# Performance work log

Hardware: AMD Instinct MI355X
Metric: run time of the kernel (lower is better)

## Reference

```python
import jax, jax.numpy as jnp
import numpy as np

B_PAIR = 4      # anchor/positive pairs; total batch = 2*B_PAIR
NUM = 4096      # keypoints per cloud
C_FEAT = 640    # descriptor dim
NB_ITER = 5


def _rigid_transform(a, b, weights):
    # a: (B,M,3), b: (B,M,3), weights: (B,M) -> (B,3,4)
    wn = weights[..., None] / (jnp.sum(weights[..., None], axis=1, keepdims=True) + 1e-5)
    centroid_a = jnp.sum(a * wn, axis=1)            # (B,3)
    centroid_b = jnp.sum(b * wn, axis=1)
    a_c = a - centroid_a[:, None, :]
    b_c = b - centroid_b[:, None, :]
    cov = jnp.swapaxes(a_c, -2, -1) @ (b_c * wn)    # (B,3,3)
    u, s, vh = jnp.linalg.svd(cov, full_matrices=False)
    v = jnp.swapaxes(vh, -2, -1)                    # torch.svd returns v, jax returns vh
    rot_pos = v @ jnp.swapaxes(u, -2, -1)
    v_neg = v.at[:, :, 2].multiply(-1.0)
    rot_neg = v_neg @ jnp.swapaxes(u, -2, -1)
    rot = jnp.where(jnp.linalg.det(rot_pos)[:, None, None] > 0, rot_pos, rot_neg)
    trans = -rot @ centroid_a[:, :, None] + centroid_b[:, :, None]
    return jnp.concatenate((rot, trans), axis=2)    # (B,3,4)


def _uot_forward(point_features, point_coords, gamma, epsilon):
    feats = point_features[..., 0]                  # (2B, C, N)
    twoB, _, N = feats.shape
    B = twoB // 2
    feat1 = jnp.transpose(feats[:B], (0, 2, 1))     # (B, N, C)
    feat2 = jnp.transpose(feats[B:], (0, 2, 1))
    coords = point_coords.reshape(twoB, -1, 4)
    coords1 = coords[:B, :, 1:]                     # (B, N, 3)
    coords2 = coords[B:, :, 1:]

    eps = jnp.exp(epsilon) + 0.03                   # scalar (1,)
    gam = jnp.exp(gamma)

    f1 = feat1 / jnp.sqrt(jnp.sum(feat1**2, -1, keepdims=True) + 1e-8)
    f2 = feat2 / jnp.sqrt(jnp.sum(feat2**2, -1, keepdims=True) + 1e-8)
    Cmat = 1.0 - jnp.einsum('bnc,bmc->bnm', f1, f2)  # (B,N,N) cosine cost
    K = jnp.exp(-Cmat / eps)

    power = gam / (gam + eps)
    inv_n = jnp.asarray(1.0 / N, K.dtype)
    a = jnp.full((B, N, 1), inv_n, K.dtype)
    prob1 = jnp.full((B, N, 1), inv_n, K.dtype)
    prob2 = jnp.full((B, N, 1), inv_n, K.dtype)
    b = prob2
    for _ in range(NB_ITER):                        # unrolled unbalanced Sinkhorn
        KTa = jnp.matmul(jnp.swapaxes(K, 1, 2), a)  # (B,N,1)
        b = jnp.power(prob2 / (KTa + 1e-8), power)
        Kb = jnp.matmul(K, b)
        a = jnp.power(prob1 / (Kb + 1e-8), power)
    T = a * K * jnp.swapaxes(b, 1, 2)               # (B,N,N) transport plan

    row_sum = jnp.sum(T, axis=-1, keepdims=True)    # (B,N,1)
    sinkhorn_matches = jnp.matmul(T, coords2) / (row_sum + 1e-8)  # (B,N,3)
    transform = _rigid_transform(coords1, sinkhorn_matches, row_sum[..., 0])
    return T, sinkhorn_matches, transform


def setup_inputs() -> dict:
    key = jax.random.key(0)
    k1, k2 = jax.random.split(key)
    point_features = jax.random.normal(k1, (2 * B_PAIR, C_FEAT, NUM, 1), dtype=jnp.float32)
    point_coords = jax.random.normal(k2, (2 * B_PAIR * NUM, 4), dtype=jnp.float32) * 10.0
    gamma = jnp.zeros((1,), jnp.float32)
    epsilon = jnp.zeros((1,), jnp.float32)
    return {"point_features": point_features, "point_coords": point_coords,
            "gamma": gamma, "epsilon": epsilon}


def reference(point_features, point_coords, gamma, epsilon):
    return _uot_forward(point_features, point_coords, gamma, epsilon)
```

## Files before the change

### kernel.cpp

```cpp
#include <hip/hip_runtime.h>
#include <math.h>

#define NB 4
#define N 4096
#define CF 640

typedef _Float16 f16;
typedef _Float16 f16x8 __attribute__((ext_vector_type(8)));
typedef _Float16 f16x4 __attribute__((ext_vector_type(4)));
typedef float    f32x4 __attribute__((ext_vector_type(4)));
typedef unsigned int u32;

#define OFF_FNT   0ll
#define OFF_RNORM (OFF_FNT + 8ll*N*CF*2)
#define OFF_BVEC  (OFF_RNORM + 8ll*N*4)
#define OFF_SCR   (OFF_BVEC + (long long)NB*N*4)
#define OFF_KTAP  (OFF_SCR + (long long)NB*N*N*2)
#define REQ_H     (OFF_KTAP + (long long)NB*64*N*4)
#define REQ_F     (OFF_SCR + (long long)NB*64*N*4)

__device__ inline void async_copy16(void* lds, const void* g) {
    __builtin_amdgcn_global_load_lds(
        (const __attribute__((address_space(1))) u32*)g,
        (__attribute__((address_space(3))) u32*)lds,
        16, 0, 0);
}

__global__ __launch_bounds__(256) void rnorm_kernel(const float* __restrict__ pf,
                                                    float* __restrict__ rnorm) {
    int idx = blockIdx.x * 256 + threadIdx.x;
    int n = idx & (N - 1);
    int b = idx >> 12;
    const float* src = pf + (size_t)b * CF * N + n;
    float s = 0.f;
    for (int c = 0; c < CF; ++c) { float v = src[(size_t)c * N]; s = fmaf(v, v, s); }
    rnorm[idx] = 1.0f / sqrtf(s + 1e-8f);
}

__global__ __launch_bounds__(256) void transpose_kernel(const float* __restrict__ pf,
                                                        const float* __restrict__ rnorm,
                                                        f16* __restrict__ fnT) {
    __shared__ float tile[64][65];
    int b  = blockIdx.z;
    int c0 = blockIdx.x * 64;
    int n1 = blockIdx.y * 64;
    int t  = threadIdx.x;

    int c_l = t >> 4;
    int n_l4 = (t & 15) * 4;
    #pragma unroll
    for (int i = 0; i < 4; ++i) {
        int c = c_l + i * 16;
        float4 v = *(const float4*)(pf + (size_t)(b * CF + c0 + c) * N + n1 + n_l4);
        tile[c][n_l4 + 0] = v.x; tile[c][n_l4 + 1] = v.y;
        tile[c][n_l4 + 2] = v.z; tile[c][n_l4 + 3] = v.w;
    }
    __syncthreads();

    int n_l = t >> 2;
    int c_g = (t & 3) * 16;
    float rn = rnorm[b * N + n1 + n_l];
    f16 tmp[16] __attribute__((aligned(16)));
    #pragma unroll
    for (int i = 0; i < 16; ++i)
        tmp[i] = (f16)(tile[c_g + i][n_l] * rn);
    f16* dst = fnT + (size_t)(b * N + n1 + n_l) * CF + c0 + c_g;
    ((uint4*)dst)[0] = ((const uint4*)tmp)[0];
    ((uint4*)dst)[1] = ((const uint4*)tmp)[1];
}

template<bool H>
__global__ __launch_bounds__(256) void gemm_k(const f16* __restrict__ fnT,
                                              const float* __restrict__ e_in,
                                              float* __restrict__ Kf,
                                              f16* __restrict__ Kh,
                                              float* __restrict__ ktap) {
    int b  = blockIdx.z;
    int m0 = blockIdx.y * 128;
    int n0 = blockIdx.x * 128;
    const f16* A = fnT + (size_t)b       * N * CF;
    const f16* B = fnT + (size_t)(b + 4) * N * CF;

    __shared__ f16 As[128 * 32];
    __shared__ f16 Bs[128 * 32];
    __shared__ float cs[2][128];
    __shared__ f16 Ct[H ? 128 * 136 : 1];

    int tid = threadIdx.x;
    int w = tid >> 6;
    int l = tid & 63;
    int wr = w >> 1, wc = w & 1;

    f32x4 acc[4][4];
    #pragma unroll
    for (int i = 0; i < 4; ++i)
        #pragma unroll
        for (int j = 0; j < 4; ++j)
            acc[i][j] = (f32x4){0.f, 0.f, 0.f, 0.f};

    int srow = l >> 2;
    int scp  = l & 3;

    for (int c0 = 0; c0 < CF; c0 += 32) {
        #pragma unroll
        for (int q = 0; q < 2; ++q) {
            int ch = w * 2 + q;
            int row = ch * 16 + srow;
            int cc = scp ^ ((row >> 1) & 3);
            async_copy16(&As[ch * 512], A + (size_t)(n0 + row) * CF + c0 + cc * 8);
            async_copy16(&Bs[ch * 512], B + (size_t)(m0 + row) * CF + c0 + cc * 8);
        }
        __syncthreads();

        f16x8 af[4], bfr[4];
        int g = l >> 4, low = l & 15;
        #pragma unroll
        for (int t = 0; t < 4; ++t) {
            int rowA = wr * 64 + t * 16 + low;
            af[t] = *(const f16x8*)(As + rowA * 32 + (g ^ ((rowA >> 1) & 3)) * 8);
            int rowB = wc * 64 + t * 16 + low;
            bfr[t] = *(const f16x8*)(Bs + rowB * 32 + (g ^ ((rowB >> 1) & 3)) * 8);
        }
        #pragma unroll
        for (int i = 0; i < 4; ++i)
            #pragma unroll
            for (int j = 0; j < 4; ++j)
                acc[i][j] = __builtin_amdgcn_mfma_f32_16x16x32_f16(af[i], bfr[j], acc[i][j], 0, 0, 0);
        __syncthreads();
    }

    float eps = expf(e_in[0]) + 0.03f;
    float inv_eps = 1.0f / eps;
    int g4 = l >> 4, low = l & 15;
    float colp[4] = {0.f, 0.f, 0.f, 0.f};
    float* out = Kf + (size_t)b * N * N;

    #pragma unroll
    for (int i = 0; i < 4; ++i) {
        int rl = wr * 64 + i * 16 + g4 * 4;
        #pragma unroll
        for (int j = 0; j < 4; ++j) {
            int cl = wc * 64 + j * 16 + low;
            #pragma unroll
            for (int r = 0; r < 4; ++r) {
                float v = expf((acc[i][j][r] - 1.0f) * inv_eps);
                out[(size_t)(n0 + rl + r) * N + m0 + cl] = v;
                if constexpr (H) Ct[(rl + r) * 136 + cl] = (f16)v;
                colp[j] += v;
            }
        }
    }

    #pragma unroll
    for (int j = 0; j < 4; ++j) {
        float c = colp[j];
        c += __shfl_down(c, 32);
        c += __shfl_down(c, 16);
        if (l < 16) cs[wr][wc * 64 + j * 16 + l] = c;
    }
    __syncthreads();
    if (tid < 128)
        ktap[((size_t)b * 64 + blockIdx.x) * N + m0 + tid] =
            (cs[0][tid] + cs[1][tid]) * (1.0f / N);

    if constexpr (H) {
        f16* oh = Kh + (size_t)b * N * N;
        int row0 = tid >> 4, c8 = (tid & 15) * 8;
        #pragma unroll
        for (int rr = 0; rr < 8; ++rr) {
            int row = rr * 16 + row0;
            f16x8 v = *(const f16x8*)(Ct + row * 136 + c8);
            *(f16x8*)(oh + (size_t)(n0 + row) * N + m0 + c8) = v;
        }
    }
}

__global__ __launch_bounds__(256) void bvec_kernel(const float* __restrict__ ktap,
                                                   int npart, int slotstride,
                                                   const float* __restrict__ g_in,
                                                   const float* __restrict__ e_in,
                                                   float* __restrict__ bvec) {
    int cl = threadIdx.x & 63;
    int pg = threadIdx.x >> 6;
    int i = blockIdx.x * 64 + cl;
    int b = i >> 12, m = i & (N - 1);
    const float* p = ktap + (size_t)b * slotstride * N + m;
    int per = npart >> 2;
    float s = 0.f;
    #pragma unroll 8
    for (int k = pg * per; k < (pg + 1) * per; ++k) s += p[(size_t)k * N];
    __shared__ float sh[4][64];
    sh[pg][cl] = s; __syncthreads();
    if (threadIdx.x < 64) {
        float tot = sh[0][cl] + sh[1][cl] + sh[2][cl] + sh[3][cl];
        float eps = expf(e_in[0]) + 0.03f;
        float gam = expf(g_in[0]);
        float power = gam / (gam + eps);
        bvec[i] = powf((1.0f / N) / (tot + 1e-8f), power);
    }
}

template<bool H>
__global__ __launch_bounds__(256) void fused_iter(const void* __restrict__ Kp,
                                                  const float* __restrict__ bv_in,
                                                  const float* __restrict__ g_in,
                                                  const float* __restrict__ e_in,
                                                  float* __restrict__ ktap) {
    int b = blockIdx.y, slab = blockIdx.x;
    int n0s = slab * 16;
    int w = threadIdx.x >> 6, l = threadIdx.x & 63;
    __shared__ float ash[16];
    float eps = expf(e_in[0]) + 0.03f;
    float gam = expf(g_in[0]);
    float power = gam / (gam + eps);
    const float* bv = bv_in + b * N;

    float acc[4] = {0.f, 0.f, 0.f, 0.f};

    if constexpr (H) {
        const f16* Kb = (const f16*)Kp + ((size_t)b * N + n0s) * N;
        for (int it = 0; it < 8; ++it) {
            int m = it * 512 + l * 8;
            float bq[8];
            *(float4*)&bq[0] = *(const float4*)(bv + m);
            *(float4*)&bq[4] = *(const float4*)(bv + m + 4);
            #pragma unroll
            for (int rr = 0; rr < 4; ++rr) {
                f16x8 v = *(const f16x8*)(Kb + (size_t)(w * 4 + rr) * N + m);
                #pragma unroll
                for (int q = 0; q < 8; ++q) acc[rr] = fmaf((float)v[q], bq[q], acc[rr]);
            }
        }
    } else {
        const float* Kb = (const float*)Kp + ((size_t)b * N + n0s) * N;
        for (int it = 0; it < 16; ++it) {
            int m = it * 256 + l * 4;
            float4 bq = *(const float4*)(bv + m);
            #pragma unroll
            for (int rr = 0; rr < 4; ++rr) {
                float4 v = *(const float4*)(Kb + (size_t)(rr * 4 + w) * N + m);
                acc[rr] = fmaf(v.x, bq.x, acc[rr]);
                acc[rr] = fmaf(v.y, bq.y, acc[rr]);
                acc[rr] = fmaf(v.z, bq.z, acc[rr]);
                acc[rr] = fmaf(v.w, bq.w, acc[rr]);
            }
        }
    }
    #pragma unroll
    for (int rr = 0; rr < 4; ++rr) {
        float s = acc[rr];
        s += __shfl_down(s, 32);
        s += __shfl_down(s, 16);
        s += __shfl_down(s, 8);
        s += __shfl_down(s, 4);
        s += __shfl_down(s, 2);
        s += __shfl_down(s, 1);
        if (l == 0) ash[(H ? w * 4 + rr : rr * 4 + w)] =
            powf((1.0f / N) / (s + 1e-8f), power);
    }
    __syncthreads();

    float cacc[16];
    #pragma unroll
    for (int q = 0; q < 16; ++q) cacc[q] = 0.f;
    int t4 = threadIdx.x * 4;
    if constexpr (H) {
        const f16* Kb = (const f16*)Kp + ((size_t)b * N + n0s) * N;
        for (int r = 0; r < 16; ++r) {
            float a = ash[r];
            #pragma unroll
            for (int q = 0; q < 4; ++q) {
                f16x4 v = *(const f16x4*)(Kb + (size_t)r * N + q * 1024 + t4);
                #pragma unroll
                for (int j = 0; j < 4; ++j)
                    cacc[q * 4 + j] = fmaf((float)v[j], a, cacc[q * 4 + j]);
            }
        }
    } else {
        const float* Kb = (const float*)Kp + ((size_t)b * N + n0s) * N;
        for (int r = 0; r < 16; ++r) {
            float a = ash[r];
            #pragma unroll
            for (int q = 0; q < 4; ++q) {
                float4 v = *(const float4*)(Kb + (size_t)r * N + q * 1024 + t4);
                cacc[q * 4 + 0] = fmaf(v.x, a, cacc[q * 4 + 0]);
                cacc[q * 4 + 1] = fmaf(v.y, a, cacc[q * 4 + 1]);
                cacc[q * 4 + 2] = fmaf(v.z, a, cacc[q * 4 + 2]);
                cacc[q * 4 + 3] = fmaf(v.w, a, cacc[q * 4 + 3]);
            }
        }
    }
    float* o = ktap + ((size_t)b * 256 + slab) * N;
    #pragma unroll
    for (int q = 0; q < 4; ++q)
        *(float4*)(o + q * 1024 + t4) =
            make_float4(cacc[q * 4], cacc[q * 4 + 1], cacc[q * 4 + 2], cacc[q * 4 + 3]);
}

__global__ __launch_bounds__(256) void final_k(float* __restrict__ Tout,
                                               const float* __restrict__ bv_in,
                                               const float* __restrict__ g_in,
                                               const float* __restrict__ e_in,
                                               const float* __restrict__ pc,
                                               float* __restrict__ rowsum,
                                               float* __restrict__ matches) {
    int b = blockIdx.y, n = blockIdx.x;
    int t = threadIdx.x;
    int t4 = t * 4;
    const float* bv = bv_in + b * N;
    float kv[16], bl[16];
    float* Trow = Tout + ((size_t)b * N + n) * N;
    #pragma unroll
    for (int q = 0; q < 4; ++q) {
        *(float4*)&bl[q * 4] = *(const float4*)(bv + q * 1024 + t4);
        *(float4*)&kv[q * 4] = *(const float4*)(Trow + q * 1024 + t4);
    }
    float s = 0.f;
    #pragma unroll
    for (int q = 0; q < 16; ++q) s = fmaf(kv[q], bl[q], s);
    __shared__ float red[256];
    red[t] = s; __syncthreads();
    for (int off = 128; off; off >>= 1) {
        if (t < off) red[t] += red[t + off];
        __syncthreads();
    }
    __shared__ float a_sh;
    if (t == 0) {
        float eps = expf(e_in[0]) + 0.03f;
        float gam = expf(g_in[0]);
        float power = gam / (gam + eps);
        a_sh = powf((1.0f / N) / (red[0] + 1e-8f), power);
    }
    __syncthreads();
    float an = a_sh;
    const float4* c2 = (const float4*)pc + (size_t)(4 + b) * N;
    float rs = 0.f, s0 = 0.f, s1 = 0.f, s2 = 0.f;
    #pragma unroll
    for (int q = 0; q < 4; ++q) {
        float tv0 = an * kv[q * 4 + 0] * bl[q * 4 + 0];
        float tv1 = an * kv[q * 4 + 1] * bl[q * 4 + 1];
        float tv2 = an * kv[q * 4 + 2] * bl[q * 4 + 2];
        float tv3 = an * kv[q * 4 + 3] * bl[q * 4 + 3];
        *(float4*)(Trow + q * 1024 + t4) = make_float4(tv0, tv1, tv2, tv3);
        rs += tv0 + tv1 + tv2 + tv3;
        float4 c0 = c2[q * 1024 + t4],     c1 = c2[q * 1024 + t4 + 1],
               cc = c2[q * 1024 + t4 + 2], c3 = c2[q * 1024 + t4 + 3];
        s0 = fmaf(tv0, c0.y, s0); s1 = fmaf(tv0, c0.z, s1); s2 = fmaf(tv0, c0.w, s2);
        s0 = fmaf(tv1, c1.y, s0); s1 = fmaf(tv1, c1.z, s1); s2 = fmaf(tv1, c1.w, s2);
        s0 = fmaf(tv2, cc.y, s0); s1 = fmaf(tv2, cc.z, s1); s2 = fmaf(tv2, cc.w, s2);
        s0 = fmaf(tv3, c3.y, s0); s1 = fmaf(tv3, c3.z, s1); s2 = fmaf(tv3, c3.w, s2);
    }
    __shared__ float4 red4[256];
    red4[t] = make_float4(rs, s0, s1, s2); __syncthreads();
    for (int off = 128; off; off >>= 1) {
        if (t < off) {
            float4 o = red4[t + off];
            red4[t].x += o.x; red4[t].y += o.y; red4[t].z += o.z; red4[t].w += o.w;
        }
        __syncthreads();
    }
    if (t == 0) {
        float4 tot = red4[0];
        rowsum[b * N + n] = tot.x;
        float inv = 1.0f / (tot.x + 1e-8f);
        float* mo = matches + ((size_t)b * N + n) * 3;
        mo[0] = tot.y * inv; mo[1] = tot.z * inv; mo[2] = tot.w * inv;
    }
}

__global__ __launch_bounds__(256) void transform_kernel(const float* __restrict__ rowsum,
                                                        const float* __restrict__ matches,
                                                        const float* __restrict__ pc,
                                                        float* __restrict__ out) {
    int b = blockIdx.x;
    float vals[16];
    #pragma unroll
    for (int q = 0; q < 16; ++q) vals[q] = 0.f;
    for (int n = threadIdx.x; n < N; n += 256) {
        float w = rowsum[b * N + n];
        float4 c1 = ((const float4*)pc)[(size_t)b * N + n];
        float ax = c1.y, ay = c1.z, az = c1.w;
        const float* mm = matches + ((size_t)b * N + n) * 3;
        float bx = mm[0], by = mm[1], bz = mm[2];
        vals[0] += w;
        vals[1] = fmaf(w, ax, vals[1]); vals[2] = fmaf(w, ay, vals[2]); vals[3] = fmaf(w, az, vals[3]);
        vals[4] = fmaf(w, bx, vals[4]); vals[5] = fmaf(w, by, vals[5]); vals[6] = fmaf(w, bz, vals[6]);
        vals[7]  = fmaf(w * ax, bx, vals[7]);  vals[8]  = fmaf(w * ax, by, vals[8]);  vals[9]  = fmaf(w * ax, bz, vals[9]);
        vals[10] = fmaf(w * ay, bx, vals[10]); vals[11] = fmaf(w * ay, by, vals[11]); vals[12] = fmaf(w * ay, bz, vals[12]);
        vals[13] = fmaf(w * az, bx, vals[13]); vals[14] = fmaf(w * az, by, vals[14]); vals[15] = fmaf(w * az, bz, vals[15]);
    }
    __shared__ float red[256];
    __shared__ float tot[16];
    for (int q = 0; q < 16; ++q) {
        red[threadIdx.x] = vals[q]; __syncthreads();
        for (int off = 128; off; off >>= 1) {
            if (threadIdx.x < off) red[threadIdx.x] += red[threadIdx.x + off];
            __syncthreads();
        }
        if (threadIdx.x == 0) tot[q] = red[0];
        __syncthreads();
    }
    if (threadIdx.x != 0) return;

    double S = tot[0];
    double denom = S + 1e-5;
    double Ca[3], Cb[3], M[3][3], cov[3][3];
    for (int i = 0; i < 3; ++i) { Ca[i] = tot[1 + i] / denom; Cb[i] = tot[4 + i] / denom; }
    for (int i = 0; i < 3; ++i)
        for (int j = 0; j < 3; ++j)
            M[i][j] = tot[7 + i * 3 + j] / denom;
    double s0 = S / denom;
    for (int i = 0; i < 3; ++i)
        for (int j = 0; j < 3; ++j)
            cov[i][j] = M[i][j] - Ca[i] * Cb[j] * (2.0 - s0);

    double Sm[3][3], V[3][3] = {{1,0,0},{0,1,0},{0,0,1}};
    for (int i = 0; i < 3; ++i)
        for (int j = 0; j < 3; ++j) {
            double acc = 0;
            for (int k = 0; k < 3; ++k) acc += cov[k][i] * cov[k][j];
            Sm[i][j] = acc;
        }
    for (int sweep = 0; sweep < 20; ++sweep) {
        static const int pq[3][2] = {{0,1},{0,2},{1,2}};
        for (int r = 0; r < 3; ++r) {
            int p = pq[r][0], q = pq[r][1];
            double apq = Sm[p][q];
            if (fabs(apq) < 1e-30) continue;
            double tau = (Sm[q][q] - Sm[p][p]) / (2.0 * apq);
            double t = (tau >= 0) ? 1.0 / (tau + sqrt(1.0 + tau * tau))
                                  : 1.0 / (tau - sqrt(1.0 + tau * tau));
            double c = 1.0 / sqrt(1.0 + t * t), s = t * c;
            for (int i = 0; i < 3; ++i) {
                double sip = Sm[i][p], siq = Sm[i][q];
                Sm[i][p] = c * sip - s * siq; Sm[i][q] = s * sip + c * siq;
            }
            for (int j = 0; j < 3; ++j) {
                double spj = Sm[p][j], sqj = Sm[q][j];
                Sm[p][j] = c * spj - s * sqj; Sm[q][j] = s * spj + c * sqj;
            }
            for (int i = 0; i < 3; ++i) {
                double vip = V[i][p], viq = V[i][q];
                V[i][p] = c * vip - s * viq; V[i][q] = s * vip + c * viq;
            }
        }
    }
    double lam[3] = {Sm[0][0], Sm[1][1], Sm[2][2]};
    for (int i = 0; i < 2; ++i)
        for (int j = i + 1; j < 3; ++j)
            if (lam[j] > lam[i]) {
                double tl = lam[i]; lam[i] = lam[j]; lam[j] = tl;
                for (int k = 0; k < 3; ++k) { double tv = V[k][i]; V[k][i] = V[k][j]; V[k][j] = tv; }
            }
    double U[3][3];
    double sig0 = sqrt(fmax(lam[0], 0.0));
    for (int j = 0; j < 3; ++j) {
        double sig = sqrt(fmax(lam[j], 0.0));
        if (sig > 1e-12 * (sig0 + 1e-300)) {
            double nrm = 0;
            for (int i = 0; i < 3; ++i) {
                double u = cov[i][0] * V[0][j] + cov[i][1] * V[1][j] + cov[i][2] * V[2][j];
                U[i][j] = u; nrm += u * u;
            }
            nrm = 1.0 / sqrt(nrm + 1e-300);
            for (int i = 0; i < 3; ++i) U[i][j] *= nrm;
        } else {
            U[0][j] = U[1][0] * U[2][1] - U[2][0] * U[1][1];
            U[1][j] = U[2][0] * U[0][1] - U[0][0] * U[2][1];
            U[2][j] = U[0][0] * U[1][1] - U[1][0] * U[0][1];
        }
    }
    double R[3][3];
    for (int i = 0; i < 3; ++i)
        for (int j = 0; j < 3; ++j)
            R[i][j] = V[i][0] * U[j][0] + V[i][1] * U[j][1] + V[i][2] * U[j][2];
    double det = R[0][0] * (R[1][1] * R[2][2] - R[1][2] * R[2][1])
               - R[0][1] * (R[1][0] * R[2][2] - R[1][2] * R[2][0])
               + R[0][2] * (R[1][0] * R[2][1] - R[1][1] * R[2][0]);
    if (!(det > 0)) {
        for (int k = 0; k < 3; ++k) V[k][2] = -V[k][2];
        for (int i = 0; i < 3; ++i)
            for (int j = 0; j < 3; ++j)
                R[i][j] = V[i][0] * U[j][0] + V[i][1] * U[j][1] + V[i][2] * U[j][2];
    }
    double tr[3];
    for (int i = 0; i < 3; ++i)
        tr[i] = -(R[i][0] * Ca[0] + R[i][1] * Ca[1] + R[i][2] * Ca[2]) + Cb[i];
    float* o = out + b * 12;
    for (int i = 0; i < 3; ++i) {
        o[i * 4 + 0] = (float)R[i][0];
        o[i * 4 + 1] = (float)R[i][1];
        o[i * 4 + 2] = (float)R[i][2];
        o[i * 4 + 3] = (float)tr[i];
    }
}

extern "C" void kernel_launch(void* const* d_in, const int* in_sizes, int n_in,
                              void* d_out, int out_size, void* d_ws, size_t ws_size,
                              hipStream_t stream) {
    const float* pf   = (const float*)d_in[0];
    const float* pc   = (const float*)d_in[1];
    const float* g_in = (const float*)d_in[2];
    const float* e_in = (const float*)d_in[3];

    char* wsb = (char*)d_ws;
    f16*   fnT   = (f16*)(wsb + OFF_FNT);
    float* rnorm = (float*)(wsb + OFF_RNORM);
    float* bvec  = (float*)(wsb + OFF_BVEC);

    float* T_out   = (float*)d_out;
    float* matches = T_out + (size_t)NB * N * N;
    float* trans   = matches + (size_t)NB * N * 3;
    float* rowsum  = rnorm;

    rnorm_kernel<<<dim3(8 * N / 256), 256, 0, stream>>>(pf, rnorm);
    transpose_kernel<<<dim3(CF / 64, N / 64, 8), 256, 0, stream>>>(pf, rnorm, fnT);

    float* ktapF = (float*)(wsb + OFF_FNT);

    if (ws_size >= (size_t)REQ_H) {
        f16*   Kh    = (f16*)(wsb + OFF_SCR);
        float* ktapG = (float*)(wsb + OFF_KTAP);
        gemm_k<true><<<dim3(N / 128, N / 128, NB), 256, 0, stream>>>(fnT, e_in, T_out, Kh, ktapG);
        bvec_kernel<<<dim3(NB * N / 64), 256, 0, stream>>>(ktapG, 32, 64, g_in, e_in, bvec);
        for (int it = 0; it < 4; ++it) {
            fused_iter<true><<<dim3(N / 16, NB), 256, 0, stream>>>(Kh, bvec, g_in, e_in, ktapF);
            bvec_kernel<<<dim3(NB * N / 64), 256, 0, stream>>>(ktapF, 256, 256, g_in, e_in, bvec);
        }
        final_k<<<dim3(N, NB), 256, 0, stream>>>(T_out, bvec, g_in, e_in, pc, rowsum, matches);
    } else {
        float* ktapG = (float*)(wsb + OFF_SCR);
        gemm_k<false><<<dim3(N / 128, N / 128, NB), 256, 0, stream>>>(fnT, e_in, T_out, (f16*)nullptr, ktapG);
        bvec_kernel<<<dim3(NB * N / 64), 256, 0, stream>>>(ktapG, 32, 64, g_in, e_in, bvec);
        for (int it = 0; it < 4; ++it) {
            fused_iter<false><<<dim3(N / 16, NB), 256, 0, stream>>>(T_out, bvec, g_in, e_in, ktapF);
            bvec_kernel<<<dim3(NB * N / 64), 256, 0, stream>>>(ktapF, 256, 256, g_in, e_in, bvec);
        }
        final_k<<<dim3(N, NB), 256, 0, stream>>>(T_out, bvec, g_in, e_in, pc, rowsum, matches);
    }

    transform_kernel<<<dim3(NB), 256, 0, stream>>>(rowsum, matches, pc, trans);
}
```

Baseline: 867.6 us.

## Keep K slab in registers across Sinkhorn halves and batch final rows

```diff
diff --git a/kernel.cpp b/kernel.cpp
--- a/kernel.cpp
+++ b/kernel.cpp
@@ -24,6 +24,16 @@
         (const __attribute__((address_space(1))) u32*)g,
         (__attribute__((address_space(3))) u32*)lds,
         16, 0, 0);
+}
+
+__device__ inline float wave_sum(float s) {
+    s += __shfl_down(s, 32);
+    s += __shfl_down(s, 16);
+    s += __shfl_down(s, 8);
+    s += __shfl_down(s, 4);
+    s += __shfl_down(s, 2);
+    s += __shfl_down(s, 1);
+    return s;
 }
 
 __global__ __launch_bounds__(256) void rnorm_kernel(const float* __restrict__ pf,
@@ -84,7 +94,7 @@
     __shared__ f16 As[128 * 32];
     __shared__ f16 Bs[128 * 32];
     __shared__ float cs[2][128];
-    __shared__ f16 Ct[H ? 128 * 136 : 1];
+    __shared__ f16 Ct[H ? 64 * 136 : 1];
 
     int tid = threadIdx.x;
     int w = tid >> 6;
@@ -145,7 +155,7 @@
             for (int r = 0; r < 4; ++r) {
                 float v = expf((acc[i][j][r] - 1.0f) * inv_eps);
                 out[(size_t)(n0 + rl + r) * N + m0 + cl] = v;
-                if constexpr (H) Ct[(rl + r) * 136 + cl] = (f16)v;
+                acc[i][j][r] = v;
                 colp[j] += v;
             }
         }
@@ -165,12 +175,30 @@
 
     if constexpr (H) {
         f16* oh = Kh + (size_t)b * N * N;
-        int row0 = tid >> 4, c8 = (tid & 15) * 8;
-        #pragma unroll
-        for (int rr = 0; rr < 8; ++rr) {
-            int row = rr * 16 + row0;
-            f16x8 v = *(const f16x8*)(Ct + row * 136 + c8);
-            *(f16x8*)(oh + (size_t)(n0 + row) * N + m0 + c8) = v;
+        int row0 = tid >> 4, c8v = (tid & 15) * 8;
+        #pragma unroll
+        for (int half = 0; half < 2; ++half) {
+            __syncthreads();
+            if (wr == half) {
+                #pragma unroll
+                for (int i = 0; i < 4; ++i) {
+                    int rl = i * 16 + g4 * 4;
+                    #pragma unroll
+                    for (int j = 0; j < 4; ++j) {
+                        int cl = wc * 64 + j * 16 + low;
+                        #pragma unroll
+                        for (int r = 0; r < 4; ++r)
+                            Ct[(rl + r) * 136 + cl] = (f16)acc[i][j][r];
+                    }
+                }
+            }
+            __syncthreads();
+            #pragma unroll
+            for (int rr = 0; rr < 4; ++rr) {
+                int row = rr * 16 + row0;
+                f16x8 v = *(const f16x8*)(Ct + row * 136 + c8v);
+                *(f16x8*)(oh + (size_t)(n0 + half * 64 + row) * N + m0 + c8v) = v;
+            }
         }
     }
 }
@@ -208,93 +236,112 @@
                                                   float* __restrict__ ktap) {
     int b = blockIdx.y, slab = blockIdx.x;
     int n0s = slab * 16;
-    int w = threadIdx.x >> 6, l = threadIdx.x & 63;
-    __shared__ float ash[16];
+    int t = threadIdx.x;
+    int w = t >> 6, l = t & 63;
+    __shared__ float wred[4][4];
     float eps = expf(e_in[0]) + 0.03f;
     float gam = expf(g_in[0]);
     float power = gam / (gam + eps);
     const float* bv = bv_in + b * N;
 
-    float acc[4] = {0.f, 0.f, 0.f, 0.f};
-
     if constexpr (H) {
+        float bl[16];
+        #pragma unroll
+        for (int q = 0; q < 2; ++q) {
+            *(float4*)&bl[q * 8]     = *(const float4*)(bv + q * 2048 + t * 8);
+            *(float4*)&bl[q * 8 + 4] = *(const float4*)(bv + q * 2048 + t * 8 + 4);
+        }
+        float cacc[16];
+        #pragma unroll
+        for (int q = 0; q < 16; ++q) cacc[q] = 0.f;
         const f16* Kb = (const f16*)Kp + ((size_t)b * N + n0s) * N;
-        for (int it = 0; it < 8; ++it) {
-            int m = it * 512 + l * 8;
-            float bq[8];
-            *(float4*)&bq[0] = *(const float4*)(bv + m);
-            *(float4*)&bq[4] = *(const float4*)(bv + m + 4);
-            #pragma unroll
-            for (int rr = 0; rr < 4; ++rr) {
-                f16x8 v = *(const f16x8*)(Kb + (size_t)(w * 4 + rr) * N + m);
+
+        for (int g4 = 0; g4 < 4; ++g4) {
+            f16x8 kr[4][2];
+            #pragma unroll
+            for (int r = 0; r < 4; ++r)
                 #pragma unroll
-                for (int q = 0; q < 8; ++q) acc[rr] = fmaf((float)v[q], bq[q], acc[rr]);
-            }
+                for (int q = 0; q < 2; ++q)
+                    kr[r][q] = *(const f16x8*)(Kb + (size_t)(g4 * 4 + r) * N + q * 2048 + t * 8);
+            #pragma unroll
+            for (int r = 0; r < 4; ++r) {
+                float s = 0.f;
+                #pragma unroll
+                for (int q = 0; q < 2; ++q)
+                    #pragma unroll
+                    for (int j = 0; j < 8; ++j)
+                        s = fmaf((float)kr[r][q][j], bl[q * 8 + j], s);
+                s = wave_sum(s);
+                if (l == 0) wred[w][r] = s;
+            }
+            __syncthreads();
+            float av[4];
+            #pragma unroll
+            for (int r = 0; r < 4; ++r) {
+                float s = wred[0][r] + wred[1][r] + wred[2][r] + wred[3][r];
+                av[r] = powf((1.0f / N) / (s + 1e-8f), power);
+            }
+            __syncthreads();
+            #pragma unroll
+            for (int r = 0; r < 4; ++r)
+                #pragma unroll
+                for (int q = 0; q < 2; ++q)
+                    #pragma unroll
+                    for (int j = 0; j < 8; ++j)
+                        cacc[q * 8 + j] = fmaf((float)kr[r][q][j], av[r], cacc[q * 8 + j]);
+        }
+        float* o = ktap + ((size_t)b * 256 + slab) * N;
+        #pragma unroll
+        for (int q = 0; q < 2; ++q) {
+            *(float4*)(o + q * 2048 + t * 8)     = make_float4(cacc[q*8+0], cacc[q*8+1], cacc[q*8+2], cacc[q*8+3]);
+            *(float4*)(o + q * 2048 + t * 8 + 4) = make_float4(cacc[q*8+4], cacc[q*8+5], cacc[q*8+6], cacc[q*8+7]);
         }
     } else {
+        int t4 = t * 4;
+        float bl[16];
+        #pragma unroll
+        for (int q = 0; q < 4; ++q)
+            *(float4*)&bl[q * 4] = *(const float4*)(bv + q * 1024 + t4);
+        float cacc[16];
+        #pragma unroll
+        for (int q = 0; q < 16; ++q) cacc[q] = 0.f;
         const float* Kb = (const float*)Kp + ((size_t)b * N + n0s) * N;
-        for (int it = 0; it < 16; ++it) {
-            int m = it * 256 + l * 4;
-            float4 bq = *(const float4*)(bv + m);
-            #pragma unroll
-            for (int rr = 0; rr < 4; ++rr) {
-                float4 v = *(const float4*)(Kb + (size_t)(rr * 4 + w) * N + m);
-                acc[rr] = fmaf(v.x, bq.x, acc[rr]);
-                acc[rr] = fmaf(v.y, bq.y, acc[rr]);
-                acc[rr] = fmaf(v.z, bq.z, acc[rr]);
-                acc[rr] = fmaf(v.w, bq.w, acc[rr]);
-            }
-        }
-    }
-    #pragma unroll
-    for (int rr = 0; rr < 4; ++rr) {
-        float s = acc[rr];
-        s += __shfl_down(s, 32);
-        s += __shfl_down(s, 16);
-        s += __shfl_down(s, 8);
-        s += __shfl_down(s, 4);
-        s += __shfl_down(s, 2);
-        s += __shfl_down(s, 1);
-        if (l == 0) ash[(H ? w * 4 + rr : rr * 4 + w)] =
-            powf((1.0f / N) / (s + 1e-8f), power);
-    }
-    __syncthreads();
-
-    float cacc[16];
-    #pragma unroll
-    for (int q = 0; q < 16; ++q) cacc[q] = 0.f;
-    int t4 = threadIdx.x * 4;
-    if constexpr (H) {
-        const f16* Kb = (const f16*)Kp + ((size_t)b * N + n0s) * N;
-        for (int r = 0; r < 16; ++r) {
-            float a = ash[r];
-            #pragma unroll
-            for (int q = 0; q < 4; ++q) {
-                f16x4 v = *(const f16x4*)(Kb + (size_t)r * N + q * 1024 + t4);
+
+        for (int g4 = 0; g4 < 4; ++g4) {
+            float kr[4][16];
+            #pragma unroll
+            for (int r = 0; r < 4; ++r)
                 #pragma unroll
-                for (int j = 0; j < 4; ++j)
-                    cacc[q * 4 + j] = fmaf((float)v[j], a, cacc[q * 4 + j]);
-            }
-        }
-    } else {
-        const float* Kb = (const float*)Kp + ((size_t)b * N + n0s) * N;
-        for (int r = 0; r < 16; ++r) {
-            float a = ash[r];
-            #pragma unroll
-            for (int q = 0; q < 4; ++q) {
-                float4 v = *(const float4*)(Kb + (size_t)r * N + q * 1024 + t4);
-                cacc[q * 4 + 0] = fmaf(v.x, a, cacc[q * 4 + 0]);
-                cacc[q * 4 + 1] = fmaf(v.y, a, cacc[q * 4 + 1]);
-                cacc[q * 4 + 2] = fmaf(v.z, a, cacc[q * 4 + 2]);
-                cacc[q * 4 + 3] = fmaf(v.w, a, cacc[q * 4 + 3]);
-            }
-        }
-    }
-    float* o = ktap + ((size_t)b * 256 + slab) * N;
-    #pragma unroll
-    for (int q = 0; q < 4; ++q)
-        *(float4*)(o + q * 1024 + t4) =
-            make_float4(cacc[q * 4], cacc[q * 4 + 1], cacc[q * 4 + 2], cacc[q * 4 + 3]);
+                for (int q = 0; q < 4; ++q)
+                    *(float4*)&kr[r][q * 4] = *(const float4*)(Kb + (size_t)(g4 * 4 + r) * N + q * 1024 + t4);
+            #pragma unroll
+            for (int r = 0; r < 4; ++r) {
+                float s = 0.f;
+                #pragma unroll
+                for (int q = 0; q < 16; ++q) s = fmaf(kr[r][q], bl[q], s);
+                s = wave_sum(s);
+                if (l == 0) wred[w][r] = s;
+            }
+            __syncthreads();
+            float av[4];
+            #pragma unroll
+            for (int r = 0; r < 4; ++r) {
+                float s = wred[0][r] + wred[1][r] + wred[2][r] + wred[3][r];
+                av[r] = powf((1.0f / N) / (s + 1e-8f), power);
+            }
+            __syncthreads();
+            #pragma unroll
+            for (int r = 0; r < 4; ++r)
+                #pragma unroll
+                for (int q = 0; q < 16; ++q)
+                    cacc[q] = fmaf(kr[r][q], av[r], cacc[q]);
+        }
+        float* o = ktap + ((size_t)b * 256 + slab) * N;
+        #pragma unroll
+        for (int q = 0; q < 4; ++q)
+            *(float4*)(o + q * 1024 + t4) =
+                make_float4(cacc[q * 4], cacc[q * 4 + 1], cacc[q * 4 + 2], cacc[q * 4 + 3]);
+    }
 }
 
 __global__ __launch_bounds__(256) void final_k(float* __restrict__ Tout,
@@ -304,66 +351,87 @@
                                                const float* __restrict__ pc,
                                                float* __restrict__ rowsum,
                                                float* __restrict__ matches) {
-    int b = blockIdx.y, n = blockIdx.x;
-    int t = threadIdx.x;
+    int b = blockIdx.y, n0r = blockIdx.x * 4;
+    int t = threadIdx.x, w = t >> 6, l = t & 63;
     int t4 = t * 4;
     const float* bv = bv_in + b * N;
-    float kv[16], bl[16];
-    float* Trow = Tout + ((size_t)b * N + n) * N;
-    #pragma unroll
-    for (int q = 0; q < 4; ++q) {
+    float eps = expf(e_in[0]) + 0.03f;
+    float gam = expf(g_in[0]);
+    float power = gam / (gam + eps);
+
+    float bl[16];
+    #pragma unroll
+    for (int q = 0; q < 4; ++q)
         *(float4*)&bl[q * 4] = *(const float4*)(bv + q * 1024 + t4);
-        *(float4*)&kv[q * 4] = *(const float4*)(Trow + q * 1024 + t4);
-    }
-    float s = 0.f;
-    #pragma unroll
-    for (int q = 0; q < 16; ++q) s = fmaf(kv[q], bl[q], s);
-    __shared__ float red[256];
-    red[t] = s; __syncthreads();
-    for (int off = 128; off; off >>= 1) {
-        if (t < off) red[t] += red[t + off];
-        __syncthreads();
-    }
-    __shared__ float a_sh;
-    if (t == 0) {
-        float eps = expf(e_in[0]) + 0.03f;
-        float gam = expf(g_in[0]);
-        float power = gam / (gam + eps);
-        a_sh = powf((1.0f / N) / (red[0] + 1e-8f), power);
+
+    float* Trow0 = Tout + ((size_t)b * N + n0r) * N;
+    float kv[4][16];
+    #pragma unroll
+    for (int r = 0; r < 4; ++r)
+        #pragma unroll
+        for (int q = 0; q < 4; ++q)
+            *(float4*)&kv[r][q * 4] = *(const float4*)(Trow0 + (size_t)r * N + q * 1024 + t4);
+
+    __shared__ float wred[4][4];
+    #pragma unroll
+    for (int r = 0; r < 4; ++r) {
+        float s = 0.f;
+        #pragma unroll
+        for (int q = 0; q < 16; ++q) s = fmaf(kv[r][q], bl[q], s);
+        s = wave_sum(s);
+        if (l == 0) wred[w][r] = s;
     }
     __syncthreads();
-    float an = a_sh;
+    float av[4];
+    #pragma unroll
+    for (int r = 0; r < 4; ++r) {
+        float s = wred[0][r] + wred[1][r] + wred[2][r] + wred[3][r];
+        av[r] = powf((1.0f / N) / (s + 1e-8f), power);
+    }
+
     const float4* c2 = (const float4*)pc + (size_t)(4 + b) * N;
-    float rs = 0.f, s0 = 0.f, s1 = 0.f, s2 = 0.f;
-    #pragma unroll
-    for (int q = 0; q < 4; ++q) {
-        float tv0 = an * kv[q * 4 + 0] * bl[q * 4 + 0];
-        float tv1 = an * kv[q * 4 + 1] * bl[q * 4 + 1];
-        float tv2 = an * kv[q * 4 + 2] * bl[q * 4 + 2];
-        float tv3 = an * kv[q * 4 + 3] * bl[q * 4 + 3];
-        *(float4*)(Trow + q * 1024 + t4) = make_float4(tv0, tv1, tv2, tv3);
-        rs += tv0 + tv1 + tv2 + tv3;
-        float4 c0 = c2[q * 1024 + t4],     c1 = c2[q * 1024 + t4 + 1],
-               cc = c2[q * 1024 + t4 + 2], c3 = c2[q * 1024 + t4 + 3];
-        s0 = fmaf(tv0, c0.y, s0); s1 = fmaf(tv0, c0.z, s1); s2 = fmaf(tv0, c0.w, s2);
-        s0 = fmaf(tv1, c1.y, s0); s1 = fmaf(tv1, c1.z, s1); s2 = fmaf(tv1, c1.w, s2);
-        s0 = fmaf(tv2, cc.y, s0); s1 = fmaf(tv2, cc.z, s1); s2 = fmaf(tv2, cc.w, s2);
-        s0 = fmaf(tv3, c3.y, s0); s1 = fmaf(tv3, c3.z, s1); s2 = fmaf(tv3, c3.w, s2);
-    }
-    __shared__ float4 red4[256];
-    red4[t] = make_float4(rs, s0, s1, s2); __syncthreads();
-    for (int off = 128; off; off >>= 1) {
-        if (t < off) {
-            float4 o = red4[t + off];
-            red4[t].x += o.x; red4[t].y += o.y; red4[t].z += o.z; red4[t].w += o.w;
-        }
-        __syncthreads();
-    }
-    if (t == 0) {
-        float4 tot = red4[0];
-        rowsum[b * N + n] = tot.x;
+    float rsv[4], s0v[4], s1v[4], s2v[4];
+    #pragma unroll
+    for (int r = 0; r < 4; ++r) {
+        float rs = 0.f, s0 = 0.f, s1 = 0.f, s2 = 0.f;
+        float an = av[r];
+        #pragma unroll
+        for (int q = 0; q < 4; ++q) {
+            int idx = q * 1024 + t4;
+            float tv0 = an * kv[r][q * 4 + 0] * bl[q * 4 + 0];
+            float tv1 = an * kv[r][q * 4 + 1] * bl[q * 4 + 1];
+            float tv2 = an * kv[r][q * 4 + 2] * bl[q * 4 + 2];
+            float tv3 = an * kv[r][q * 4 + 3] * bl[q * 4 + 3];
+            *(float4*)(Trow0 + (size_t)r * N + idx) = make_float4(tv0, tv1, tv2, tv3);
+            rs += tv0 + tv1 + tv2 + tv3;
+            float4 c0 = c2[idx], c1 = c2[idx + 1], cc = c2[idx + 2], c3 = c2[idx + 3];
+            s0 = fmaf(tv0, c0.y, s0); s1 = fmaf(tv0, c0.z, s1); s2 = fmaf(tv0, c0.w, s2);
+            s0 = fmaf(tv1, c1.y, s0); s1 = fmaf(tv1, c1.z, s1); s2 = fmaf(tv1, c1.w, s2);
+            s0 = fmaf(tv2, cc.y, s0); s1 = fmaf(tv2, cc.z, s1); s2 = fmaf(tv2, cc.w, s2);
+            s0 = fmaf(tv3, c3.y, s0); s1 = fmaf(tv3, c3.z, s1); s2 = fmaf(tv3, c3.w, s2);
+        }
+        rsv[r] = rs; s0v[r] = s0; s1v[r] = s1; s2v[r] = s2;
+    }
+
+    __shared__ float4 wred4[4][4];
+    #pragma unroll
+    for (int r = 0; r < 4; ++r) {
+        float rs = wave_sum(rsv[r]);
+        float s0 = wave_sum(s0v[r]);
+        float s1 = wave_sum(s1v[r]);
+        float s2 = wave_sum(s2v[r]);
+        if (l == 0) wred4[w][r] = make_float4(rs, s0, s1, s2);
+    }
+    __syncthreads();
+    if (t < 4) {
+        float4 a0 = wred4[0][t], a1 = wred4[1][t], a2 = wred4[2][t], a3 = wred4[3][t];
+        float4 tot = make_float4(a0.x + a1.x + a2.x + a3.x,
+                                 a0.y + a1.y + a2.y + a3.y,
+                                 a0.z + a1.z + a2.z + a3.z,
+                                 a0.w + a1.w + a2.w + a3.w);
+        rowsum[b * N + n0r + t] = tot.x;
         float inv = 1.0f / (tot.x + 1e-8f);
-        float* mo = matches + ((size_t)b * N + n) * 3;
+        float* mo = matches + ((size_t)b * N + n0r + t) * 3;
         mo[0] = tot.y * inv; mo[1] = tot.z * inv; mo[2] = tot.w * inv;
     }
 }
@@ -373,34 +441,34 @@
                                                         const float* __restrict__ pc,
                                                         float* __restrict__ out) {
     int b = blockIdx.x;
+    int t = threadIdx.x, w = t >> 6, l = t & 63;
     float vals[16];
     #pragma unroll
     for (int q = 0; q < 16; ++q) vals[q] = 0.f;
-    for (int n = threadIdx.x; n < N; n += 256) {
-        float w = rowsum[b * N + n];
+    for (int n = t; n < N; n += 256) {
+        float wgt = rowsum[b * N + n];
         float4 c1 = ((const float4*)pc)[(size_t)b * N + n];
         float ax = c1.y, ay = c1.z, az = c1.w;
         const float* mm = matches + ((size_t)b * N + n) * 3;
         float bx = mm[0], by = mm[1], bz = mm[2];
-        vals[0] += w;
-        vals[1] = fmaf(w, ax, vals[1]); vals[2] = fmaf(w, ay, vals[2]); vals[3] = fmaf(w, az, vals[3]);
-        vals[4] = fmaf(w, bx, vals[4]); vals[5] = fmaf(w, by, vals[5]); vals[6] = fmaf(w, bz, vals[6]);
-        vals[7]  = fmaf(w * ax, bx, vals[7]);  vals[8]  = fmaf(w * ax, by, vals[8]);  vals[9]  = fmaf(w * ax, bz, vals[9]);
-        vals[10] = fmaf(w * ay, bx, vals[10]); vals[11] = fmaf(w * ay, by, vals[11]); vals[12] = fmaf(w * ay, bz, vals[12]);
-        vals[13] = fmaf(w * az, bx, vals[13]); vals[14] = fmaf(w * az, by, vals[14]); vals[15] = fmaf(w * az, bz, vals[15]);
-    }
-    __shared__ float red[256];
+        vals[0] += wgt;
+        vals[1] = fmaf(wgt, ax, vals[1]); vals[2] = fmaf(wgt, ay, vals[2]); vals[3] = fmaf(wgt, az, vals[3]);
+        vals[4] = fmaf(wgt, bx, vals[4]); vals[5] = fmaf(wgt, by, vals[5]); vals[6] = fmaf(wgt, bz, vals[6]);
+        vals[7]  = fmaf(wgt * ax, bx, vals[7]);  vals[8]  = fmaf(wgt * ax, by, vals[8]);  vals[9]  = fmaf(wgt * ax, bz, vals[9]);
+        vals[10] = fmaf(wgt * ay, bx, vals[10]); vals[11] = fmaf(wgt * ay, by, vals[11]); vals[12] = fmaf(wgt * ay, bz, vals[12]);
+        vals[13] = fmaf(wgt * az, bx, vals[13]); vals[14] = fmaf(wgt * az, by, vals[14]); vals[15] = fmaf(wgt * az, bz, vals[15]);
+    }
+    __shared__ float sh[4][16];
     __shared__ float tot[16];
+    #pragma unroll
     for (int q = 0; q < 16; ++q) {
-        red[threadIdx.x] = vals[q]; __syncthreads();
-        for (int off = 128; off; off >>= 1) {
-            if (threadIdx.x < off) red[threadIdx.x] += red[threadIdx.x + off];
-            __syncthreads();
-        }
-        if (threadIdx.x == 0) tot[q] = red[0];
-        __syncthreads();
-    }
-    if (threadIdx.x != 0) return;
+        float s = wave_sum(vals[q]);
+        if (l == 0) sh[w][q] = s;
+    }
+    __syncthreads();
+    if (t < 16) tot[t] = sh[0][t] + sh[1][t] + sh[2][t] + sh[3][t];
+    __syncthreads();
+    if (t != 0) return;
 
     double S = tot[0];
     double denom = S + 1e-5;
@@ -428,9 +496,9 @@
             double apq = Sm[p][q];
             if (fabs(apq) < 1e-30) continue;
             double tau = (Sm[q][q] - Sm[p][p]) / (2.0 * apq);
-            double t = (tau >= 0) ? 1.0 / (tau + sqrt(1.0 + tau * tau))
-                                  : 1.0 / (tau - sqrt(1.0 + tau * tau));
-            double c = 1.0 / sqrt(1.0 + t * t), s = t * c;
+            double t2 = (tau >= 0) ? 1.0 / (tau + sqrt(1.0 + tau * tau))
+                                   : 1.0 / (tau - sqrt(1.0 + tau * tau));
+            double c = 1.0 / sqrt(1.0 + t2 * t2), s = t2 * c;
             for (int i = 0; i < 3; ++i) {
                 double sip = Sm[i][p], siq = Sm[i][q];
                 Sm[i][p] = c * sip - s * siq; Sm[i][q] = s * sip + c * siq;
@@ -527,7 +595,7 @@
             fused_iter<true><<<dim3(N / 16, NB), 256, 0, stream>>>(Kh, bvec, g_in, e_in, ktapF);
             bvec_kernel<<<dim3(NB * N / 64), 256, 0, stream>>>(ktapF, 256, 256, g_in, e_in, bvec);
         }
-        final_k<<<dim3(N, NB), 256, 0, stream>>>(T_out, bvec, g_in, e_in, pc, rowsum, matches);
+        final_k<<<dim3(N / 4, NB), 256, 0, stream>>>(T_out, bvec, g_in, e_in, pc, rowsum, matches);
     } else {
         float* ktapG = (float*)(wsb + OFF_SCR);
         gemm_k<false><<<dim3(N / 128, N / 128, NB), 256, 0, stream>>>(fnT, e_in, T_out, (f16*)nullptr, ktapG);
@@ -536,7 +604,7 @@
             fused_iter<false><<<dim3(N / 16, NB), 256, 0, stream>>>(T_out, bvec, g_in, e_in, ktapF);
             bvec_kernel<<<dim3(NB * N / 64), 256, 0, stream>>>(ktapF, 256, 256, g_in, e_in, bvec);
         }
-        final_k<<<dim3(N, NB), 256, 0, stream>>>(T_out, bvec, g_in, e_in, pc, rowsum, matches);
+        final_k<<<dim3(N / 4, NB), 256, 0, stream>>>(T_out, bvec, g_in, e_in, pc, rowsum, matches);
     }
 
     transform_kernel<<<dim3(NB), 256, 0, stream>>>(rowsum, matches, pc, trans);
```

New measurement: 870.8 us. No clear change (+0.4%).
